# Optimization experiments

Measured on AMD Instinct MI355X. Metric: run time of the kernel, lower is better.

## Reference

```python
import jax, jax.numpy as jnp
import numpy as np

NUM_LEVELS = 10      # multi-resolution levels
FEATURES = 2         # features per level
TABLE_SIZE = 2 ** 16 # hash table entries per level (power of 2)
MIN_RES = 16
MAX_RES = 512
NET_WIDTH = 64
PRIMES = jnp.array([1, 2654435761, 805459861], dtype=jnp.uint32)


def _grid_sizes():
    g = np.exp(np.linspace(np.log(MIN_RES), np.log(MAX_RES), NUM_LEVELS))
    return np.round(g).astype(np.float32)


# [8,3] binary corner offsets of a voxel
_OFFSETS = jnp.array([[i, j, k] for i in (0, 1) for j in (0, 1) for k in (0, 1)],
                     dtype=jnp.uint32)


def hash_encode(positions, table):
    """positions [N,3] in [0,1]; table [L,T,F] -> [N, L*F]."""
    grid_sizes = jnp.asarray(_grid_sizes(), dtype=positions.dtype)  # [L]

    def one_level(table_l, n):
        scaled = positions * n                      # [N,3]
        floor = jnp.floor(scaled)
        frac = scaled - floor                        # [N,3]
        base = floor.astype(jnp.uint32)              # [N,3]
        corners = base[:, None, :] + _OFFSETS[None]  # [N,8,3]
        h = corners * PRIMES                         # uint32 overflow-wrapping mul
        idx = (h[..., 0] ^ h[..., 1] ^ h[..., 2]) & jnp.uint32(TABLE_SIZE - 1)  # [N,8]
        feats = table_l[idx]                         # gather: [N,8,F]
        off_f = _OFFSETS[None].astype(frac.dtype)    # [1,8,3]
        w = jnp.prod(jnp.where(off_f > 0, frac[:, None, :], 1.0 - frac[:, None, :]),
                     axis=-1)                        # trilinear weights [N,8]
        return jnp.sum(feats * w[..., None], axis=1) # [N,F]

    feats = jax.vmap(one_level, in_axes=(0, 0), out_axes=1)(table, grid_sizes)  # [N,L,F]
    return feats.reshape(positions.shape[0], -1)


def setup_inputs() -> dict:
    key = jax.random.key(0)
    k_pos, k_tab, k_w1, k_w2 = jax.random.split(key, 4)
    N = 1048576
    positions = jax.random.uniform(k_pos, (N, 3), dtype=jnp.float32)
    # hash tables init small uniform (Instant-NGP style)
    table = jax.random.uniform(k_tab, (NUM_LEVELS, TABLE_SIZE, FEATURES),
                               dtype=jnp.float32, minval=-1e-4, maxval=1e-4)
    d_in = NUM_LEVELS * FEATURES
    # he_uniform init
    lim1 = np.sqrt(6.0 / d_in)
    W1 = jax.random.uniform(k_w1, (d_in, NET_WIDTH), jnp.float32, -lim1, lim1)
    b1 = jnp.zeros((NET_WIDTH,), jnp.float32)
    lim2 = np.sqrt(6.0 / NET_WIDTH)
    W2 = jax.random.uniform(k_w2, (NET_WIDTH, 1), jnp.float32, -lim2, lim2)
    b2 = jnp.zeros((1,), jnp.float32)
    return {"positions": positions, "table": table, "W1": W1, "b1": b1,
            "W2": W2, "b2": b2}


def reference(positions, table, W1, b1, W2, b2):
    x = hash_encode(positions, table)              # [N, L*F]
    x = jax.nn.relu(x @ W1 + b1)                   # [N, 64]
    density = x @ W2 + b2                          # [N, 1]
    return density
```

## Files before the change

### kernel.cpp

```cpp
#include <hip/hip_runtime.h>
#include <math.h>

#define NLEV 10
#define TSZ 65536
#define MASK (TSZ - 1)
#define P2 2654435761u
#define P3 805459861u
#define NBUCK 32768
#define QSCALE 1.0e-4f
#define DEQ (QSCALE / 32767.0f)

typedef float v2f __attribute__((ext_vector_type(2)));
typedef float v4f __attribute__((ext_vector_type(4)));

struct GS { float g[NLEV]; };


__device__ __forceinline__ float encode_mlp_packed(
    float px, float py, float pz, const unsigned* __restrict__ ptab,
    const float* __restrict__ W1, const float* __restrict__ b1,
    const float* __restrict__ W2, const float* __restrict__ b2, const GS& gs)
{
    float feats[2 * NLEV];

#pragma unroll
    for (int g = 0; g < 2; ++g) {
        unsigned raw[5][8];
        float rxs[5], rys[5], rzs[5];

#pragma unroll
        for (int li = 0; li < 5; ++li) {
            const int l = g * 5 + li;
            float n = gs.g[l];
            float sx = px * n, sy = py * n, sz = pz * n;
            float fx = floorf(sx), fy = floorf(sy), fz = floorf(sz);
            rxs[li] = sx - fx; rys[li] = sy - fy; rzs[li] = sz - fz;
            unsigned bx = (unsigned)fx, by = (unsigned)fy, bz = (unsigned)fz;

            unsigned hx0 = bx,      hx1 = bx + 1u;
            unsigned hy0 = by * P2, hy1 = hy0 + P2;
            unsigned hz0 = bz * P3, hz1 = hz0 + P3;

            const unsigned* tl = ptab + (size_t)l * TSZ;
            raw[li][0] = tl[(hx0 ^ hy0 ^ hz0) & MASK];
            raw[li][1] = tl[(hx0 ^ hy0 ^ hz1) & MASK];
            raw[li][2] = tl[(hx0 ^ hy1 ^ hz0) & MASK];
            raw[li][3] = tl[(hx0 ^ hy1 ^ hz1) & MASK];
            raw[li][4] = tl[(hx1 ^ hy0 ^ hz0) & MASK];
            raw[li][5] = tl[(hx1 ^ hy0 ^ hz1) & MASK];
            raw[li][6] = tl[(hx1 ^ hy1 ^ hz0) & MASK];
            raw[li][7] = tl[(hx1 ^ hy1 ^ hz1) & MASK];
        }

        __builtin_amdgcn_sched_barrier(0);

#pragma unroll
        for (int li = 0; li < 5; ++li) {
            const int l = g * 5 + li;
            float rx = rxs[li], ry = rys[li], rz = rzs[li];
            float wx1 = rx, wx0 = 1.f - rx;
            float wy1 = ry, wy0 = 1.f - ry;
            float wz1 = rz, wz0 = 1.f - rz;

            v2f acc = {0.f, 0.f};
#define CORNER(c, wx, wy, wz)                                  \
            {                                                  \
                unsigned u = raw[li][c];                       \
                int s0 = (int)(u << 16) >> 16;                 \
                int s1 = (int)u >> 16;                         \
                float w = (wx) * (wy) * (wz);                  \
                v2f sv; sv.x = (float)s0; sv.y = (float)s1;    \
                v2f wv; wv.x = w; wv.y = w;                    \
                acc = acc + sv * wv;                           \
            }
            CORNER(0, wx0, wy0, wz0)
            CORNER(1, wx0, wy0, wz1)
            CORNER(2, wx0, wy1, wz0)
            CORNER(3, wx0, wy1, wz1)
            CORNER(4, wx1, wy0, wz0)
            CORNER(5, wx1, wy0, wz1)
            CORNER(6, wx1, wy1, wz0)
            CORNER(7, wx1, wy1, wz1)
#undef CORNER
            feats[2 * l + 0] = acc.x * DEQ;
            feats[2 * l + 1] = acc.y * DEQ;
        }
    }

    v2f dens2 = {0.f, 0.f};
#pragma unroll
    for (int half = 0; half < 2; ++half) {
        const v2f* b1v = (const v2f*)(b1 + half * 32);
        v2f h2[16];
#pragma unroll
        for (int j = 0; j < 16; ++j) h2[j] = b1v[j];
#pragma unroll
        for (int k = 0; k < 2 * NLEV; ++k) {
            float xk = feats[k];
            v2f xk2; xk2.x = xk; xk2.y = xk;
            const v2f* w1v = (const v2f*)(W1 + k * 64 + half * 32);
#pragma unroll
            for (int j = 0; j < 16; ++j)
                h2[j] = h2[j] + xk2 * w1v[j];
        }
        const v2f* w2v = (const v2f*)(W2 + half * 32);
#pragma unroll
        for (int j = 0; j < 16; ++j) {
            v2f r;
            r.x = fmaxf(h2[j].x, 0.f);
            r.y = fmaxf(h2[j].y, 0.f);
            dens2 = dens2 + r * w2v[j];
        }
    }
    return b2[0] + dens2.x + dens2.y;
}


__device__ __forceinline__ unsigned part5(unsigned x) {
    unsigned r = (x & 1u);
    r |= (x & 2u) << 2;
    r |= (x & 4u) << 4;
    r |= (x & 8u) << 6;
    r |= (x & 16u) << 8;
    return r;
}

__device__ __forceinline__ unsigned morton_key(float px, float py, float pz) {
    unsigned cx = min(31u, (unsigned)(px * 32.f));
    unsigned cy = min(31u, (unsigned)(py * 32.f));
    unsigned cz = min(31u, (unsigned)(pz * 32.f));
    return part5(cx) | (part5(cy) << 1) | (part5(cz) << 2);
}

__device__ __forceinline__ unsigned pack_entry(v2f f) {
    const float kq = 32767.0f / QSCALE;
    int i0 = (int)rintf(fminf(fmaxf(f.x * kq, -32767.f), 32767.f));
    int i1 = (int)rintf(fminf(fmaxf(f.y * kq, -32767.f), 32767.f));
    return ((unsigned)i0 & 0xffffu) | ((unsigned)i1 << 16);
}


__global__ __launch_bounds__(256) void hist_repack_kernel(
    const float* __restrict__ pos, const float* __restrict__ tab,
    unsigned* __restrict__ ptab, unsigned* __restrict__ hist,
    unsigned* __restrict__ keyrank, int N)
{
    int i = blockIdx.x * blockDim.x + threadIdx.x;
    if (i < NLEV * TSZ) {
        v2f f = __builtin_nontemporal_load((const v2f*)tab + i);
        __builtin_nontemporal_store(pack_entry(f), &ptab[i]);
    }
    if (i >= N) return;
    unsigned key = morton_key(pos[i * 3], pos[i * 3 + 1], pos[i * 3 + 2]);
    unsigned rank = atomicAdd(&hist[key], 1u);
    __builtin_nontemporal_store(key | (rank << 15), &keyrank[i]);
}

__global__ __launch_bounds__(1024) void scan_kernel(
    const unsigned* __restrict__ hist, unsigned* __restrict__ bases)
{
    __shared__ unsigned wsum[16];
    int t = threadIdx.x;
    int lane = t & 63, wid = t >> 6;
    unsigned local[32];
    unsigned tsum = 0;
#pragma unroll
    for (int k = 0; k < 32; ++k) { local[k] = hist[t * 32 + k]; tsum += local[k]; }
    unsigned incl = tsum;
#pragma unroll
    for (int off = 1; off < 64; off <<= 1) {
        unsigned v = __shfl_up(incl, off, 64);
        if (lane >= off) incl += v;
    }
    unsigned excl = incl - tsum;
    if (lane == 63) wsum[wid] = incl;
    __syncthreads();
    unsigned wbase = 0;
#pragma unroll
    for (int w = 0; w < 16; ++w) wbase += (w < wid) ? wsum[w] : 0u;
    unsigned base = wbase + excl;
#pragma unroll
    for (int k = 0; k < 32; ++k) { bases[t * 32 + k] = base; base += local[k]; }
}

__global__ __launch_bounds__(256) void scatter_kernel(
    const float* __restrict__ pos, const unsigned* __restrict__ keyrank,
    const unsigned* __restrict__ bases, float4* __restrict__ pos4, int N)
{
    int i = blockIdx.x * blockDim.x + threadIdx.x;
    if (i >= N) return;
    unsigned kr = __builtin_nontemporal_load(&keyrank[i]);
    unsigned key = kr & (NBUCK - 1);
    unsigned rank = kr >> 15;
    unsigned j = bases[key] + rank;
    v4f v;
    v.x = pos[i * 3]; v.y = pos[i * 3 + 1]; v.z = pos[i * 3 + 2];
    v.w = __uint_as_float((unsigned)i);
    __builtin_nontemporal_store(v, (v4f*)pos4 + j);
}

__global__ __launch_bounds__(256) void compute_sorted_kernel(
    const float4* __restrict__ pos4, const unsigned* __restrict__ ptab,
    const float* __restrict__ W1, const float* __restrict__ b1,
    const float* __restrict__ W2, const float* __restrict__ b2,
    float* __restrict__ out, int N, GS gs)
{
    int i = blockIdx.x * blockDim.x + threadIdx.x;
    if (i >= N) return;
    float4 p = pos4[i];
    unsigned id = __float_as_uint(p.w);
    out[id] = encode_mlp_packed(p.x, p.y, p.z, ptab, W1, b1, W2, b2, gs);
}


__global__ __launch_bounds__(256) void repack_kernel(
    const float* __restrict__ tab, unsigned* __restrict__ ptab, int total)
{
    int i = blockIdx.x * blockDim.x + threadIdx.x;
    if (i >= total) return;
    v2f f; f.x = tab[i * 2]; f.y = tab[i * 2 + 1];
    ptab[i] = pack_entry(f);
}

__global__ __launch_bounds__(256) void hist_kernel(
    const float* __restrict__ pos, unsigned* __restrict__ hist, int N)
{
    int i = blockIdx.x * blockDim.x + threadIdx.x;
    if (i >= N) return;
    atomicAdd(&hist[morton_key(pos[i * 3], pos[i * 3 + 1], pos[i * 3 + 2])], 1u);
}

__global__ __launch_bounds__(256) void scatter_atomic_kernel(
    const float* __restrict__ pos, unsigned* __restrict__ bases,
    float4* __restrict__ pos4, int N)
{
    int i = blockIdx.x * blockDim.x + threadIdx.x;
    if (i >= N) return;
    float px = pos[i * 3], py = pos[i * 3 + 1], pz = pos[i * 3 + 2];
    unsigned j = atomicAdd(&bases[morton_key(px, py, pz)], 1u);
    float4 v;
    v.x = px; v.y = py; v.z = pz;
    v.w = __uint_as_float((unsigned)i);
    pos4[j] = v;
}


extern "C" void kernel_launch(void* const* d_in, const int* in_sizes, int n_in,
                              void* d_out, int out_size, void* d_ws, size_t ws_size,
                              hipStream_t stream) {
    const float* pos   = (const float*)d_in[0];
    const float* table = (const float*)d_in[1];
    const float* W1    = (const float*)d_in[2];
    const float* b1    = (const float*)d_in[3];
    const float* W2    = (const float*)d_in[4];
    const float* b2    = (const float*)d_in[5];
    float* out = (float*)d_out;
    int N = in_sizes[0] / 3;

    GS gs;
    for (int l = 0; l < NLEV; ++l) {
        double t = log(16.0) + (log(512.0) - log(16.0)) * (double)l / 9.0;
        gs.g[l] = (float)round(exp(t));
    }

    int block = 256;
    int grid = (N + block - 1) / block;
    int tot = NLEV * TSZ;

    size_t off_hist = 0;
    size_t off_pos4 = off_hist + (size_t)NBUCK * 4;
    size_t off_ptab = off_pos4 + (size_t)N * 16;
    size_t off_kr   = off_ptab + (size_t)tot * 4;
    size_t need_big = off_kr + (size_t)N * 4;
    size_t need_sm  = off_kr;

    char* ws = (char*)d_ws;
    unsigned* hist    = (unsigned*)(ws + off_hist);
    float4*   pos4    = (float4*)  (ws + off_pos4);
    unsigned* ptab    = (unsigned*)(ws + off_ptab);
    unsigned* keyrank = (unsigned*)(ws + off_kr);

    if (ws_size >= need_big) {
        (void)hipMemsetAsync(hist, 0, (size_t)NBUCK * 4, stream);
        hipLaunchKernelGGL(hist_repack_kernel, dim3(grid), dim3(block), 0, stream,
                           pos, table, ptab, hist, keyrank, N);
        hipLaunchKernelGGL(scan_kernel, dim3(1), dim3(1024), 0, stream, hist, hist);
        hipLaunchKernelGGL(scatter_kernel, dim3(grid), dim3(block), 0, stream,
                           pos, keyrank, hist, pos4, N);
        hipLaunchKernelGGL(compute_sorted_kernel, dim3(grid), dim3(block), 0, stream,
                           pos4, ptab, W1, b1, W2, b2, out, N, gs);
    } else if (ws_size >= need_sm) {
        (void)hipMemsetAsync(hist, 0, (size_t)NBUCK * 4, stream);
        hipLaunchKernelGGL(repack_kernel, dim3((tot + 255) / 256), dim3(256), 0,
                           stream, table, ptab, tot);
        hipLaunchKernelGGL(hist_kernel, dim3(grid), dim3(block), 0, stream,
                           pos, hist, N);
        hipLaunchKernelGGL(scan_kernel, dim3(1), dim3(1024), 0, stream, hist, hist);
        hipLaunchKernelGGL(scatter_atomic_kernel, dim3(grid), dim3(block), 0, stream,
                           pos, hist, pos4, N);
        hipLaunchKernelGGL(compute_sorted_kernel, dim3(grid), dim3(block), 0, stream,
                           pos4, ptab, W1, b1, W2, b2, out, N, gs);
    }
}
```

Baseline: 218.0 us.

## Expand coarse hash levels into dense grids for spatially local gathers

For the seven coarsest levels, the table is expanded into a dense packed 3D grid indexed by voxel coordinates, so the corner lookups of nearby Morton-sorted points hit adjacent memory instead of scattered hash slots. The three finest levels keep the hashed packed table. The dense grid (about 25 MB) is filled inside the histogram/repack kernel with a grid-stride loop, adding extra write traffic and workspace on every call. Nontemporal load/store hints are also dropped from the existing kernels, and per-level resolutions become compile-time constants.

New measurement: 176.0 us. 19.3% less time.

```diff
diff --git a/kernel.cpp b/kernel.cpp
--- a/kernel.cpp
+++ b/kernel.cpp
@@ -10,10 +10,181 @@
 #define QSCALE 1.0e-4f
 #define DEQ (QSCALE / 32767.0f)
 
+#define DTOT 6265937
+
 typedef float v2f __attribute__((ext_vector_type(2)));
-typedef float v4f __attribute__((ext_vector_type(4)));
 
 struct GS { float g[NLEV]; };
+
+
+__device__ __forceinline__ unsigned part5(unsigned x) {
+    unsigned r = (x & 1u);
+    r |= (x & 2u) << 2;
+    r |= (x & 4u) << 4;
+    r |= (x & 8u) << 6;
+    r |= (x & 16u) << 8;
+    return r;
+}
+
+__device__ __forceinline__ unsigned morton_key(float px, float py, float pz) {
+    unsigned cx = min(31u, (unsigned)(px * 32.f));
+    unsigned cy = min(31u, (unsigned)(py * 32.f));
+    unsigned cz = min(31u, (unsigned)(pz * 32.f));
+    return part5(cx) | (part5(cy) << 1) | (part5(cz) << 2);
+}
+
+__device__ __forceinline__ unsigned pack_entry(v2f f) {
+    const float kq = 32767.0f / QSCALE;
+    int i0 = (int)rintf(fminf(fmaxf(f.x * kq, -32767.f), 32767.f));
+    int i1 = (int)rintf(fminf(fmaxf(f.y * kq, -32767.f), 32767.f));
+    return ((unsigned)i0 & 0xffffu) | ((unsigned)i1 << 16);
+}
+
+
+__device__ __forceinline__ float mlp_tail(
+    const float feats[2 * NLEV],
+    const float* __restrict__ W1, const float* __restrict__ b1,
+    const float* __restrict__ W2, const float* __restrict__ b2)
+{
+    v2f dens2 = {0.f, 0.f};
+#pragma unroll
+    for (int half = 0; half < 2; ++half) {
+        const v2f* b1v = (const v2f*)(b1 + half * 32);
+        v2f h2[16];
+#pragma unroll
+        for (int j = 0; j < 16; ++j) h2[j] = b1v[j];
+#pragma unroll
+        for (int k = 0; k < 2 * NLEV; ++k) {
+            float xk = feats[k];
+            v2f xk2; xk2.x = xk; xk2.y = xk;
+            const v2f* w1v = (const v2f*)(W1 + k * 64 + half * 32);
+#pragma unroll
+            for (int j = 0; j < 16; ++j)
+                h2[j] = h2[j] + xk2 * w1v[j];
+        }
+        const v2f* w2v = (const v2f*)(W2 + half * 32);
+#pragma unroll
+        for (int j = 0; j < 16; ++j) {
+            v2f r;
+            r.x = fmaxf(h2[j].x, 0.f);
+            r.y = fmaxf(h2[j].y, 0.f);
+            dens2 = dens2 + r * w2v[j];
+        }
+    }
+    return b2[0] + dens2.x + dens2.y;
+}
+
+#define CONSUME_LEVEL(li, l)                                           \
+    {                                                                  \
+        float rx = rxs[li], ry = rys[li], rz = rzs[li];                \
+        float wx1 = rx, wx0 = 1.f - rx;                                \
+        float wy1 = ry, wy0 = 1.f - ry;                                \
+        float wz1 = rz, wz0 = 1.f - rz;                                \
+        v2f acc = {0.f, 0.f};                                          \
+        CORNER(li, 0, wx0, wy0, wz0)                                   \
+        CORNER(li, 1, wx0, wy0, wz1)                                   \
+        CORNER(li, 2, wx0, wy1, wz0)                                   \
+        CORNER(li, 3, wx0, wy1, wz1)                                   \
+        CORNER(li, 4, wx1, wy0, wz0)                                   \
+        CORNER(li, 5, wx1, wy0, wz1)                                   \
+        CORNER(li, 6, wx1, wy1, wz0)                                   \
+        CORNER(li, 7, wx1, wy1, wz1)                                   \
+        feats[2 * (l) + 0] = acc.x * DEQ;                              \
+        feats[2 * (l) + 1] = acc.y * DEQ;                              \
+    }
+
+#define CORNER(li, c, wx, wy, wz)                                      \
+        {                                                              \
+            unsigned u = raw[li][c];                                   \
+            int s0 = (int)(u << 16) >> 16;                             \
+            int s1 = (int)u >> 16;                                     \
+            float w = (wx) * (wy) * (wz);                              \
+            v2f sv; sv.x = (float)s0; sv.y = (float)s1;                \
+            v2f wv; wv.x = w; wv.y = w;                                \
+            acc = acc + sv * wv;                                       \
+        }
+
+
+#define ISSUE_DENSE(li, R, D, OFF)                                     \
+    {                                                                  \
+        const float n = (float)(R);                                    \
+        float sx = px * n, sy = py * n, sz = pz * n;                   \
+        float fx = floorf(sx), fy = floorf(sy), fz = floorf(sz);       \
+        rxs[li] = sx - fx; rys[li] = sy - fy; rzs[li] = sz - fz;       \
+        unsigned bx = (unsigned)fx, by = (unsigned)fy, bz = (unsigned)fz; \
+        unsigned base = (OFF) + (bz * (D) + by) * (D) + bx;            \
+        raw[li][0] = dtab[base];                                       \
+        raw[li][1] = dtab[base + (D) * (D)];                           \
+        raw[li][2] = dtab[base + (D)];                                 \
+        raw[li][3] = dtab[base + (D) + (D) * (D)];                     \
+        raw[li][4] = dtab[base + 1];                                   \
+        raw[li][5] = dtab[base + 1 + (D) * (D)];                       \
+        raw[li][6] = dtab[base + 1 + (D)];                             \
+        raw[li][7] = dtab[base + 1 + (D) + (D) * (D)];                 \
+    }
+
+#define ISSUE_HASH(li, l, R)                                           \
+    {                                                                  \
+        const float n = (float)(R);                                    \
+        float sx = px * n, sy = py * n, sz = pz * n;                   \
+        float fx = floorf(sx), fy = floorf(sy), fz = floorf(sz);       \
+        rxs[li] = sx - fx; rys[li] = sy - fy; rzs[li] = sz - fz;       \
+        unsigned bx = (unsigned)fx, by = (unsigned)fy, bz = (unsigned)fz; \
+        unsigned hx0 = bx,      hx1 = bx + 1u;                         \
+        unsigned hy0 = by * P2, hy1 = hy0 + P2;                        \
+        unsigned hz0 = bz * P3, hz1 = hz0 + P3;                        \
+        const unsigned* tl = ptab + (size_t)(l) * TSZ;                 \
+        raw[li][0] = tl[(hx0 ^ hy0 ^ hz0) & MASK];                     \
+        raw[li][1] = tl[(hx0 ^ hy0 ^ hz1) & MASK];                     \
+        raw[li][2] = tl[(hx0 ^ hy1 ^ hz0) & MASK];                     \
+        raw[li][3] = tl[(hx0 ^ hy1 ^ hz1) & MASK];                     \
+        raw[li][4] = tl[(hx1 ^ hy0 ^ hz0) & MASK];                     \
+        raw[li][5] = tl[(hx1 ^ hy0 ^ hz1) & MASK];                     \
+        raw[li][6] = tl[(hx1 ^ hy1 ^ hz0) & MASK];                     \
+        raw[li][7] = tl[(hx1 ^ hy1 ^ hz1) & MASK];                     \
+    }
+
+__device__ __forceinline__ float encode_mlp_dense(
+    float px, float py, float pz,
+    const unsigned* __restrict__ dtab, const unsigned* __restrict__ ptab,
+    const float* __restrict__ W1, const float* __restrict__ b1,
+    const float* __restrict__ W2, const float* __restrict__ b2)
+{
+    float feats[2 * NLEV];
+
+    {
+        unsigned raw[5][8];
+        float rxs[5], rys[5], rzs[5];
+        ISSUE_DENSE(0, 16, 17, 0u)
+        ISSUE_DENSE(1, 24, 25, 4913u)
+        ISSUE_DENSE(2, 35, 36, 20538u)
+        ISSUE_DENSE(3, 51, 52, 67194u)
+        ISSUE_DENSE(4, 75, 76, 207802u)
+        __builtin_amdgcn_sched_barrier(0);
+        CONSUME_LEVEL(0, 0)
+        CONSUME_LEVEL(1, 1)
+        CONSUME_LEVEL(2, 2)
+        CONSUME_LEVEL(3, 3)
+        CONSUME_LEVEL(4, 4)
+    }
+    {
+        unsigned raw[5][8];
+        float rxs[5], rys[5], rzs[5];
+        ISSUE_DENSE(0, 110, 111, 646778u)
+        ISSUE_DENSE(1, 161, 162, 2014409u)
+        ISSUE_HASH(2, 7, 237)
+        ISSUE_HASH(3, 8, 348)
+        ISSUE_HASH(4, 9, 512)
+        __builtin_amdgcn_sched_barrier(0);
+        CONSUME_LEVEL(0, 5)
+        CONSUME_LEVEL(1, 6)
+        CONSUME_LEVEL(2, 7)
+        CONSUME_LEVEL(3, 8)
+        CONSUME_LEVEL(4, 9)
+    }
+
+    return mlp_tail(feats, W1, b1, W2, b2);
+}
 
 
 __device__ __forceinline__ float encode_mlp_packed(
@@ -27,7 +198,6 @@
     for (int g = 0; g < 2; ++g) {
         unsigned raw[5][8];
         float rxs[5], rys[5], rzs[5];
-
 #pragma unroll
         for (int li = 0; li < 5; ++li) {
             const int l = g * 5 + li;
@@ -36,11 +206,9 @@
             float fx = floorf(sx), fy = floorf(sy), fz = floorf(sz);
             rxs[li] = sx - fx; rys[li] = sy - fy; rzs[li] = sz - fz;
             unsigned bx = (unsigned)fx, by = (unsigned)fy, bz = (unsigned)fz;
-
             unsigned hx0 = bx,      hx1 = bx + 1u;
             unsigned hy0 = by * P2, hy1 = hy0 + P2;
             unsigned hz0 = bz * P3, hz1 = hz0 + P3;
-
             const unsigned* tl = ptab + (size_t)l * TSZ;
             raw[li][0] = tl[(hx0 ^ hy0 ^ hz0) & MASK];
             raw[li][1] = tl[(hx0 ^ hy0 ^ hz1) & MASK];
@@ -51,94 +219,56 @@
             raw[li][6] = tl[(hx1 ^ hy1 ^ hz0) & MASK];
             raw[li][7] = tl[(hx1 ^ hy1 ^ hz1) & MASK];
         }
-
         __builtin_amdgcn_sched_barrier(0);
-
 #pragma unroll
         for (int li = 0; li < 5; ++li) {
             const int l = g * 5 + li;
-            float rx = rxs[li], ry = rys[li], rz = rzs[li];
-            float wx1 = rx, wx0 = 1.f - rx;
-            float wy1 = ry, wy0 = 1.f - ry;
-            float wz1 = rz, wz0 = 1.f - rz;
-
-            v2f acc = {0.f, 0.f};
-#define CORNER(c, wx, wy, wz)                                  \
-            {                                                  \
-                unsigned u = raw[li][c];                       \
-                int s0 = (int)(u << 16) >> 16;                 \
-                int s1 = (int)u >> 16;                         \
-                float w = (wx) * (wy) * (wz);                  \
-                v2f sv; sv.x = (float)s0; sv.y = (float)s1;    \
-                v2f wv; wv.x = w; wv.y = w;                    \
-                acc = acc + sv * wv;                           \
-            }
-            CORNER(0, wx0, wy0, wz0)
-            CORNER(1, wx0, wy0, wz1)
-            CORNER(2, wx0, wy1, wz0)
-            CORNER(3, wx0, wy1, wz1)
-            CORNER(4, wx1, wy0, wz0)
-            CORNER(5, wx1, wy0, wz1)
-            CORNER(6, wx1, wy1, wz0)
-            CORNER(7, wx1, wy1, wz1)
-#undef CORNER
-            feats[2 * l + 0] = acc.x * DEQ;
-            feats[2 * l + 1] = acc.y * DEQ;
+            CONSUME_LEVEL(li, l)
         }
     }
-
-    v2f dens2 = {0.f, 0.f};
-#pragma unroll
-    for (int half = 0; half < 2; ++half) {
-        const v2f* b1v = (const v2f*)(b1 + half * 32);
-        v2f h2[16];
-#pragma unroll
-        for (int j = 0; j < 16; ++j) h2[j] = b1v[j];
-#pragma unroll
-        for (int k = 0; k < 2 * NLEV; ++k) {
-            float xk = feats[k];
-            v2f xk2; xk2.x = xk; xk2.y = xk;
-            const v2f* w1v = (const v2f*)(W1 + k * 64 + half * 32);
-#pragma unroll
-            for (int j = 0; j < 16; ++j)
-                h2[j] = h2[j] + xk2 * w1v[j];
-        }
-        const v2f* w2v = (const v2f*)(W2 + half * 32);
-#pragma unroll
-        for (int j = 0; j < 16; ++j) {
-            v2f r;
-            r.x = fmaxf(h2[j].x, 0.f);
-            r.y = fmaxf(h2[j].y, 0.f);
-            dens2 = dens2 + r * w2v[j];
-        }
-    }
-    return b2[0] + dens2.x + dens2.y;
-}
-
-
-__device__ __forceinline__ unsigned part5(unsigned x) {
-    unsigned r = (x & 1u);
-    r |= (x & 2u) << 2;
-    r |= (x & 4u) << 4;
-    r |= (x & 8u) << 6;
-    r |= (x & 16u) << 8;
-    return r;
-}
-
-__device__ __forceinline__ unsigned morton_key(float px, float py, float pz) {
-    unsigned cx = min(31u, (unsigned)(px * 32.f));
-    unsigned cy = min(31u, (unsigned)(py * 32.f));
-    unsigned cz = min(31u, (unsigned)(pz * 32.f));
-    return part5(cx) | (part5(cy) << 1) | (part5(cz) << 2);
-}
-
-__device__ __forceinline__ unsigned pack_entry(v2f f) {
-    const float kq = 32767.0f / QSCALE;
-    int i0 = (int)rintf(fminf(fmaxf(f.x * kq, -32767.f), 32767.f));
-    int i1 = (int)rintf(fminf(fmaxf(f.y * kq, -32767.f), 32767.f));
-    return ((unsigned)i0 & 0xffffu) | ((unsigned)i1 << 16);
-}
-
+    return mlp_tail(feats, W1, b1, W2, b2);
+}
+
+
+#define FILL_DENSE(lvl, D, OFF)                                        \
+    for (int d = gid; d < (D) * (D) * (D); d += gsz) {                 \
+        int zz = d / ((D) * (D));                                      \
+        int rem = d - zz * (D) * (D);                                  \
+        int yy = rem / (D);                                            \
+        int xx = rem - yy * (D);                                       \
+        unsigned h = ((unsigned)xx ^ ((unsigned)yy * P2)               \
+                      ^ ((unsigned)zz * P3)) & MASK;                   \
+        v2f f; f.x = tab[((lvl) * TSZ + h) * 2];                       \
+        f.y = tab[((lvl) * TSZ + h) * 2 + 1];                          \
+        dense[(OFF) + d] = pack_entry(f);                              \
+    }
+
+__global__ __launch_bounds__(256) void hist_repack_dense_kernel(
+    const float* __restrict__ pos, const float* __restrict__ tab,
+    unsigned* __restrict__ ptab, unsigned* __restrict__ dense,
+    unsigned* __restrict__ hist, unsigned* __restrict__ keyrank, int N)
+{
+    int gid = blockIdx.x * blockDim.x + threadIdx.x;
+    int gsz = gridDim.x * blockDim.x;
+
+    if (gid < NLEV * TSZ) {
+        v2f f; f.x = tab[gid * 2]; f.y = tab[gid * 2 + 1];
+        ptab[gid] = pack_entry(f);
+    }
+    if (gid < N) {
+        unsigned key = morton_key(pos[gid * 3], pos[gid * 3 + 1], pos[gid * 3 + 2]);
+        unsigned rank = atomicAdd(&hist[key], 1u);
+        keyrank[gid] = key | (rank << 15);
+    }
+
+    FILL_DENSE(0, 17, 0u)
+    FILL_DENSE(1, 25, 4913u)
+    FILL_DENSE(2, 36, 20538u)
+    FILL_DENSE(3, 52, 67194u)
+    FILL_DENSE(4, 76, 207802u)
+    FILL_DENSE(5, 111, 646778u)
+    FILL_DENSE(6, 162, 2014409u)
+}
 
 __global__ __launch_bounds__(256) void hist_repack_kernel(
     const float* __restrict__ pos, const float* __restrict__ tab,
@@ -147,13 +277,13 @@
 {
     int i = blockIdx.x * blockDim.x + threadIdx.x;
     if (i < NLEV * TSZ) {
-        v2f f = __builtin_nontemporal_load((const v2f*)tab + i);
-        __builtin_nontemporal_store(pack_entry(f), &ptab[i]);
+        v2f f; f.x = tab[i * 2]; f.y = tab[i * 2 + 1];
+        ptab[i] = pack_entry(f);
     }
     if (i >= N) return;
     unsigned key = morton_key(pos[i * 3], pos[i * 3 + 1], pos[i * 3 + 2]);
     unsigned rank = atomicAdd(&hist[key], 1u);
-    __builtin_nontemporal_store(key | (rank << 15), &keyrank[i]);
+    keyrank[i] = key | (rank << 15);
 }
 
 __global__ __launch_bounds__(1024) void scan_kernel(
@@ -189,14 +319,28 @@
 {
     int i = blockIdx.x * blockDim.x + threadIdx.x;
     if (i >= N) return;
-    unsigned kr = __builtin_nontemporal_load(&keyrank[i]);
+    unsigned kr = keyrank[i];
     unsigned key = kr & (NBUCK - 1);
     unsigned rank = kr >> 15;
     unsigned j = bases[key] + rank;
-    v4f v;
+    float4 v;
     v.x = pos[i * 3]; v.y = pos[i * 3 + 1]; v.z = pos[i * 3 + 2];
     v.w = __uint_as_float((unsigned)i);
-    __builtin_nontemporal_store(v, (v4f*)pos4 + j);
+    pos4[j] = v;
+}
+
+__global__ __launch_bounds__(256) void compute_sorted_dense_kernel(
+    const float4* __restrict__ pos4, const unsigned* __restrict__ dtab,
+    const unsigned* __restrict__ ptab,
+    const float* __restrict__ W1, const float* __restrict__ b1,
+    const float* __restrict__ W2, const float* __restrict__ b2,
+    float* __restrict__ out, int N)
+{
+    int i = blockIdx.x * blockDim.x + threadIdx.x;
+    if (i >= N) return;
+    float4 p = pos4[i];
+    unsigned id = __float_as_uint(p.w);
+    out[id] = encode_mlp_dense(p.x, p.y, p.z, dtab, ptab, W1, b1, W2, b2);
 }
 
 __global__ __launch_bounds__(256) void compute_sorted_kernel(
@@ -267,20 +411,32 @@
     int grid = (N + block - 1) / block;
     int tot = NLEV * TSZ;
 
-    size_t off_hist = 0;
-    size_t off_pos4 = off_hist + (size_t)NBUCK * 4;
-    size_t off_ptab = off_pos4 + (size_t)N * 16;
-    size_t off_kr   = off_ptab + (size_t)tot * 4;
-    size_t need_big = off_kr + (size_t)N * 4;
-    size_t need_sm  = off_kr;
+    size_t off_hist  = 0;
+    size_t off_pos4  = off_hist + (size_t)NBUCK * 4;
+    size_t off_ptab  = off_pos4 + (size_t)N * 16;
+    size_t off_kr    = off_ptab + (size_t)tot * 4;
+    size_t off_dense = off_kr + (size_t)N * 4;
+    size_t need_dense = off_dense + (size_t)DTOT * 4;
+    size_t need_big   = off_dense;
+    size_t need_sm    = off_kr;
 
     char* ws = (char*)d_ws;
     unsigned* hist    = (unsigned*)(ws + off_hist);
     float4*   pos4    = (float4*)  (ws + off_pos4);
     unsigned* ptab    = (unsigned*)(ws + off_ptab);
     unsigned* keyrank = (unsigned*)(ws + off_kr);
-
-    if (ws_size >= need_big) {
+    unsigned* dense   = (unsigned*)(ws + off_dense);
+
+    if (ws_size >= need_dense) {
+        (void)hipMemsetAsync(hist, 0, (size_t)NBUCK * 4, stream);
+        hipLaunchKernelGGL(hist_repack_dense_kernel, dim3(grid), dim3(block), 0,
+                           stream, pos, table, ptab, dense, hist, keyrank, N);
+        hipLaunchKernelGGL(scan_kernel, dim3(1), dim3(1024), 0, stream, hist, hist);
+        hipLaunchKernelGGL(scatter_kernel, dim3(grid), dim3(block), 0, stream,
+                           pos, keyrank, hist, pos4, N);
+        hipLaunchKernelGGL(compute_sorted_dense_kernel, dim3(grid), dim3(block), 0,
+                           stream, pos4, dense, ptab, W1, b1, W2, b2, out, N);
+    } else if (ws_size >= need_big) {
         (void)hipMemsetAsync(hist, 0, (size_t)NBUCK * 4, stream);
         hipLaunchKernelGGL(hist_repack_kernel, dim3(grid), dim3(block), 0, stream,
                            pos, table, ptab, hist, keyrank, N);
```
